# Kernel tuning notes

Hardware: AMD Instinct MI355X
Metric: run time of the kernel (lower is better)

The kernel has to match this reference:

```python
import jax, jax.numpy as jnp
import numpy as np

B, L = 2, 2048
D_MODEL = 512
KERNEL = 5
DILATIONS = (1, 2, 4, 8, 1, 2, 4, 8)
HEADS = len(DILATIONS)
HEAD_W = D_MODEL // HEADS
MODE = "center"


def _dilocal_content(x_bedl, kernel, dilations, mode):
    # x_bedl: (B, E, D, L). Returns content in layout (B, L, E, H, K, D),
    # matching LCSA's dilocal + transpose(-4,-1).transpose(-4,-2).transpose(-5,-4).
    Lx = x_bedl.shape[-1]
    per_head = []
    for d in dilations:
        P = (kernel - 1) * d
        if mode == "forward":
            pads = (P, 0)
        elif mode == "backward":
            pads = (0, P)
        else:  # center
            pads = (P // 2, P - P // 2)
        padded = jnp.pad(x_bedl, ((0, 0),) * (x_bedl.ndim - 1) + (pads,))
        win = jnp.stack([padded[..., k * d:k * d + Lx] for k in range(kernel)], axis=-2)
        per_head.append(win)
    c = jnp.stack(per_head, axis=-2)  # (B, E, D, K, H, L)
    return jnp.transpose(c, (0, 5, 1, 4, 3, 2))  # (B, L, E, H, K, D)


def setup_inputs() -> dict:
    key = jax.random.key(0)
    ks = jax.random.split(key, 6)
    s_in = 1.0 / np.sqrt(D_MODEL)
    s_out = 1.0 / np.sqrt(HEADS * HEAD_W)
    x = jax.random.normal(ks[0], (B, L, D_MODEL), jnp.float32)
    q_w = jax.random.normal(ks[1], (1, HEADS, 1, HEAD_W, D_MODEL), jnp.float32) * s_in
    q_b = jnp.zeros((1, HEADS, 1, HEAD_W), jnp.float32)
    k_w = jax.random.normal(ks[2], (1, HEADS, KERNEL, HEAD_W, D_MODEL), jnp.float32) * s_in
    k_b = jnp.zeros((1, HEADS, KERNEL, HEAD_W), jnp.float32)
    v_w = jax.random.normal(ks[3], (1, HEADS, KERNEL, HEAD_W, D_MODEL), jnp.float32) * s_in
    v_b = jnp.zeros((1, HEADS, KERNEL, HEAD_W), jnp.float32)
    o_w = jax.random.normal(ks[4], (1, D_MODEL, HEADS * HEAD_W), jnp.float32) * s_out
    o_b = jnp.zeros((1, D_MODEL), jnp.float32)
    return {"x": x, "q_w": q_w, "q_b": q_b, "k_w": k_w, "k_b": k_b,
            "v_w": v_w, "v_b": v_b, "o_w": o_w, "o_b": o_b}


def reference(x, q_w, q_b, k_w, k_b, v_w, v_b, o_w, o_b) -> jnp.ndarray:
    b, l, _ = x.shape
    # ensemble=None path: unsqueeze(-3) then transpose(-2,-1) -> (B, E=1, D, L)
    t = jnp.swapaxes(x[:, None, :, :], -2, -1)
    content = _dilocal_content(t, KERNEL, DILATIONS, MODE)  # (B, L, 1, H, K, D)
    # query uses kernel_width=1 (no padding, dilation irrelevant): (B, L, 1, H, 1, D)
    query = jnp.broadcast_to(x[:, :, None, None, None, :], (b, l, 1, HEADS, 1, D_MODEL))
    # per-(head, kernel-position) projections
    q = jnp.einsum('blehkd,ehkod->blehko', query, q_w) + q_b      # (B,L,1,H,1,O)
    k = jnp.einsum('blehkd,ehkod->blehko', content, k_w) + k_b    # (B,L,1,H,K,O)
    v = jnp.einsum('blehkd,ehkod->blehko', content, v_w) + v_b    # (B,L,1,H,K,O)
    logits = jnp.einsum('blehqo,blehko->blehqk', q, k)            # (B,L,1,H,1,K)
    score = jax.nn.softmax(logits, axis=-1)
    attn = jnp.einsum('blehqk,blehko->blehqo', score, v) / jnp.sqrt(jnp.float32(HEAD_W))
    attn = attn[..., 0, :]                                        # squeeze(-2) -> (B,L,1,H,O)
    flat = attn.reshape(b, l, 1, HEADS * HEAD_W)
    out = jnp.einsum('blef,eof->bleo', flat, o_w) + o_b           # (B,L,1,D)
    # transpose(-3,-2) then squeeze ensemble -> (B, L, D)
    return out[:, :, 0, :]
```

## Files before the change

kernel.cpp:

```cpp
#include <hip/hip_runtime.h>
#include <hip/hip_bf16.h>

using bf16 = __hip_bfloat16;
typedef __attribute__((ext_vector_type(8))) short short8;
typedef __attribute__((ext_vector_type(4))) float f32x4;

__device__ __constant__ int c_dil[8] = {1, 2, 4, 8, 1, 2, 4, 8};

__device__ inline void store1(float* p, float v) { *p = v; }
__device__ inline void store1(bf16* p, float v) { *p = __float2bfloat16(v); }

__device__ inline void gload_lds16(const void* g, void* l) {
    __builtin_amdgcn_global_load_lds(
        (const __attribute__((address_space(1))) unsigned int*)g,
        (__attribute__((address_space(3))) unsigned int*)l, 16, 0, 0);
}

template <int N> __device__ inline void vwait() {
    asm volatile("s_waitcnt vmcnt(%0)" :: "n"(N) : "memory");
    __builtin_amdgcn_sched_barrier(0);
}
__device__ inline void lgkm0_fence() {
    asm volatile("s_waitcnt lgkmcnt(0)" ::: "memory");
    __builtin_amdgcn_sched_barrier(0);
}
__device__ inline void barrier_pin() {
    __builtin_amdgcn_s_barrier();
    __builtin_amdgcn_sched_barrier(0);
}

__device__ inline unsigned short f2bf(float f) {
    const unsigned u = __float_as_uint(f);
    return (unsigned short)((u + 0x7fffu + ((u >> 16) & 1u)) >> 16);
}
__device__ inline float bf2f(unsigned short h) { return __uint_as_float(((unsigned)h) << 16); }

__device__ inline void conv_block(const float* __restrict__ src, bf16* __restrict__ dst,
                                  int ld, int mode, int idx) {
    const float4 v = *reinterpret_cast<const float4*>(src + idx);
    const int r = idx >> 9, c = idx & 511;
    bf16* d = dst + (size_t)r * ld + c;
    const float vv[4] = {v.x, v.y, v.z, v.w};
    ushort4 hi, lo;
    unsigned short* hp = &hi.x; unsigned short* lp = &lo.x;
#pragma unroll
    for (int j = 0; j < 4; ++j) {
        hp[j] = f2bf(vv[j]);
        lp[j] = f2bf(vv[j] - bf2f(hp[j]));
    }
    *reinterpret_cast<ushort4*>(d) = hi;
    if (mode == 1) *reinterpret_cast<ushort4*>(d + 512) = lo;
}

__global__ __launch_bounds__(256) void conv_all(
    const float* __restrict__ x,  const float* __restrict__ qw, const float* __restrict__ kw,
    const float* __restrict__ vw, const float* __restrict__ ow,
    const float* __restrict__ qb, const float* __restrict__ kb,
    bf16* A2, bf16* Wqk, bf16* Wv, bf16* Wo, float* bqk)
{
    const int b = blockIdx.x, t = threadIdx.x;
    if (b < 2048)       conv_block(x,  A2,                      1024, 1, (b * 256 + t) * 4);
    else if (b < 2304)  conv_block(qw, Wqk,                      512, 0, ((b - 2048) * 256 + t) * 4);
    else if (b < 3584)  conv_block(kw, Wqk + (size_t)512 * 512,  512, 0, ((b - 2304) * 256 + t) * 4);
    else if (b < 4864)  conv_block(vw, Wv,                       512, 0, ((b - 3584) * 256 + t) * 4);
    else if (b < 5120)  conv_block(ow, Wo,                       512, 0, ((b - 4864) * 256 + t) * 4);
    else { const int i = (b - 5120) * 256 + t; bqk[i] = (i < 512) ? qb[i] : kb[i - 512]; }
}

template <bool HILO>
__device__ __forceinline__ void run_gemm(
    short* smem,
    const bf16* __restrict__ A,
    const bf16* __restrict__ W,
    const float* __restrict__ bias,
    bf16* __restrict__ C, int ldc, int ncols,
    int bm, int bn)
{
    constexpr int NSTEPS = 16;
    short* Ahi = smem;
    short* Alo = smem + 8192;
    short* Bs  = smem + 16384;

    const int tid = threadIdx.x, wid = tid >> 6, lane = tid & 63;

    const int sslot = (((tid & 3) ^ ((tid >> 3) & 3)) << 4);
    const char* pAh = (const char*)A + (size_t)(bm + (tid >> 2)) * 2048 + sslot;
    const char* pB  = (const char*)W + (size_t)(bn + (tid >> 2)) * 1024 + sslot;

    auto stage = [&](int kt) {
        char* da = (char*)(Ahi + (kt & 1) * 4096);
        char* db = (char*)(Bs  + (kt & 1) * 6144);
        gload_lds16(pAh,          da + wid * 1024);
        gload_lds16(pAh + 131072, da + 4096 + wid * 1024);
        if (HILO) {
            char* dl = (char*)(Alo + (kt & 1) * 4096);
            gload_lds16(pAh + 1024,          dl + wid * 1024);
            gload_lds16(pAh + 1024 + 131072, dl + 4096 + wid * 1024);
        }
        gload_lds16(pB,           db + wid * 1024);
        gload_lds16(pB + 65536,   db + 4096 + wid * 1024);
        gload_lds16(pB + 131072,  db + 8192 + wid * 1024);
        pAh += 64; pB += 64;
    };

    f32x4 acc[4][6];
#pragma unroll
    for (int m = 0; m < 4; ++m)
#pragma unroll
        for (int n = 0; n < 6; ++n) acc[m][n] = f32x4{0.f, 0.f, 0.f, 0.f};

    const int lr16 = lane & 15;
    const int koff = (((lane >> 4) ^ ((lr16 >> 1) & 3)) << 3);
    const int wrM = wid >> 1, wcN = wid & 1;
    const int arow0 = wrM * 64 + lr16;
    const int brow0 = wcN * 96 + lr16;

    stage(0);

    for (int kt = 0; kt < NSTEPS; ++kt) {
        vwait<0>();
        barrier_pin();

        const short* ah = Ahi + (kt & 1) * 4096;
        const short* al = Alo + (kt & 1) * 4096;
        const short* bb = Bs  + (kt & 1) * 6144;
        short8 fh[4], fl[4], bw[6];
#pragma unroll
        for (int m = 0; m < 4; ++m) {
            fh[m] = *(const short8*)&ah[(arow0 + m * 16) * 32 + koff];
            if (HILO) fl[m] = *(const short8*)&al[(arow0 + m * 16) * 32 + koff];
        }
#pragma unroll
        for (int n = 0; n < 6; ++n)
            bw[n] = *(const short8*)&bb[(brow0 + n * 16) * 32 + koff];
        lgkm0_fence();
        barrier_pin();

        if (kt + 1 < NSTEPS) stage(kt + 1);

        __builtin_amdgcn_s_setprio(1);
#pragma unroll
        for (int m = 0; m < 4; ++m)
#pragma unroll
            for (int n = 0; n < 6; ++n)
                acc[m][n] = __builtin_amdgcn_mfma_f32_16x16x32_bf16(fh[m], bw[n], acc[m][n], 0, 0, 0);
        if (HILO) {
#pragma unroll
            for (int m = 0; m < 4; ++m)
#pragma unroll
                for (int n = 0; n < 6; ++n)
                    acc[m][n] = __builtin_amdgcn_mfma_f32_16x16x32_bf16(fl[m], bw[n], acc[m][n], 0, 0, 0);
        }
        __builtin_amdgcn_s_setprio(0);
    }

    const int r4 = (lane >> 4) * 4;
#pragma unroll
    for (int m = 0; m < 4; ++m) {
#pragma unroll
        for (int n = 0; n < 6; ++n) {
            const int col = bn + wcN * 96 + n * 16 + lr16;
            if (col < ncols) {
                const float bv = bias[col];
#pragma unroll
                for (int jj = 0; jj < 4; ++jj) {
                    const int row = bm + wrM * 64 + m * 16 + r4 + jj;
                    store1(C + (size_t)row * ldc + col, acc[m][n][jj] + bv);
                }
            }
        }
    }
}

__global__ __launch_bounds__(256, 2) void gemm_qkv(
    const bf16* __restrict__ A,
    const bf16* __restrict__ Wqk, const float* __restrict__ bqk, bf16* __restrict__ PQK,
    const bf16* __restrict__ Wv,  const float* __restrict__ vb,  bf16* __restrict__ PV)
{
    __shared__ short smem[28672];
    const int b = blockIdx.x;
    if (b < 512) {
        const int xcd = b & 7, i = b >> 3;
        const int by = xcd * 4 + (i & 3), bx = i >> 2;
        run_gemm<true>(smem, A, Wqk, bqk, PQK, 3072, 3072, by * 128, bx * 192);
    } else {
        const int v = b - 512;
        const int xcd = v & 7, i = v >> 3;
        const int by = xcd * 4 + (i & 3), bx = i >> 2;
        run_gemm<false>(smem, A, Wv, vb, PV, 2560, 2560, by * 128, bx * 192);
    }
}

template <int BN, typename TC>
__global__ __launch_bounds__(256) void gemm128(
    const bf16* __restrict__ A, int lda, int cw, int rpx,
    const bf16* __restrict__ W0, int ldw0, const float* __restrict__ b0,
    TC* __restrict__ C0, int ldc0, int nt0, int nx0)
{
    constexpr int NF = BN / 32;
    constexpr int NLOAD = (BN == 128) ? 4 : 3;
    __shared__ short As[4][128 * 32];
    __shared__ short Bs[4][BN * 32];

    const int tid = threadIdx.x, wid = tid >> 6, lane = tid & 63;

    const int xcd = (int)blockIdx.x & 7;
    const int i   = (int)blockIdx.x >> 3;
    const int grp = rpx * cw;
    const int cc = i / grp, w2 = i % grp;
    const int rr = w2 / cw, c = w2 % cw;
    const int bx = cc * cw + c;
    const int by = xcd * rpx + rr;

    const int bm = by * 128;
    const int bn = bx * BN;
    const int nsteps = nt0;

    const int srow = lane >> 2;
    const int ssw  = (((lane & 3) ^ ((lane >> 3) & 3)) << 4);
    const char* pA0 = (const char*)A + (size_t)(bm + wid * 16 + srow) * lda * 2 + ssw;
    const char* pA1 = pA0 + (size_t)64 * lda * 2;
    const char* pB0 = (const char*)W0 + (size_t)(bn + wid * 16 + srow) * ldw0 * 2 + ssw;

    f32x4 acc[4][NF];
#pragma unroll
    for (int m = 0; m < 4; ++m)
#pragma unroll
        for (int n = 0; n < NF; ++n) acc[m][n] = f32x4{0.f, 0.f, 0.f, 0.f};

    const int lr16 = lane & 15;
    const int wsw8 = (((lane >> 4) ^ ((lr16 >> 1) & 3)) << 3);
    const int wr = wid >> 1, wc = wid & 1;
    int offA[4], offB[NF];
#pragma unroll
    for (int m = 0; m < 4; ++m) offA[m] = (wr * 4 + m) * 512 + lr16 * 32 + wsw8;
#pragma unroll
    for (int n = 0; n < NF; ++n) offB[n] = (wc * NF + n) * 512 + lr16 * 32 + wsw8;

    auto stage = [&](int buf) {
        gload_lds16(pA0, (char*)As[buf] + wid * 1024);
        gload_lds16(pA1, (char*)As[buf] + (wid + 4) * 1024);
        gload_lds16(pB0, (char*)Bs[buf] + wid * 1024);
        pA0 += 64; pA1 += 64; pB0 += 64;
    };

    stage(0);
    stage(1);
    stage(2);

    for (int s = 0; s < nsteps; ++s) {
        const int cur = s & 3;
        if (s + 3 < nsteps) {
            stage((s + 3) & 3);
            vwait<3 * NLOAD>();
        } else if (s + 2 < nsteps) {
            vwait<2 * NLOAD>();
        } else if (s + 1 < nsteps) {
            vwait<NLOAD>();
        } else {
            vwait<0>();
        }
        barrier_pin();

        short8 af[4], bw[NF];
#pragma unroll
        for (int m = 0; m < 4; ++m)
            af[m] = *(const short8*)&As[cur][offA[m]];
#pragma unroll
        for (int n = 0; n < NF; ++n)
            bw[n] = *(const short8*)&Bs[cur][offB[n]];

        __builtin_amdgcn_s_setprio(1);
#pragma unroll
        for (int m = 0; m < 4; ++m)
#pragma unroll
            for (int n = 0; n < NF; ++n)
                acc[m][n] = __builtin_amdgcn_mfma_f32_16x16x32_bf16(af[m], bw[n], acc[m][n], 0, 0, 0);
        __builtin_amdgcn_s_setprio(0);

        barrier_pin();
    }

    const int r4 = (lane >> 4) * 4;
#pragma unroll
    for (int m = 0; m < 4; ++m) {
#pragma unroll
        for (int n = 0; n < NF; ++n) {
            const int col = bn + wc * (NF * 16) + n * 16 + lr16;
            const float bv = b0[col];
#pragma unroll
            for (int jj = 0; jj < 4; ++jj) {
                const int row = bm + wr * 64 + m * 16 + r4 + jj;
                store1(C0 + (size_t)row * ldc0 + col, acc[m][n][jj] + bv);
            }
        }
    }
}

__global__ __launch_bounds__(256) void attn_k(
    const bf16* __restrict__ PQK, const bf16* __restrict__ PV, bf16* __restrict__ Aout)
{
    const int lane = threadIdx.x & 63;
    const int wave = threadIdx.x >> 6;
    const int task = blockIdx.x * 4 + wave;
    const int h  = task & 7;
    const int bl = task >> 3;
    const int l  = bl & 2047;
    const int d  = c_dil[h];

    const float q = __bfloat162float(PQK[(size_t)bl * 3072 + h * 64 + lane]);

    float logits[5], vvals[5];
#pragma unroll
    for (int kk = 0; kk < 5; ++kk) {
        const int pos = l + (kk - 2) * d;
        const bool ok = (pos >= 0) && (pos < 2048);
        float kv = 0.f, vv = 0.f;
        if (ok) {
            const size_t rb = (size_t)(bl - l + pos);
            kv = __bfloat162float(PQK[rb * 3072 + 512 + (h * 5 + kk) * 64 + lane]);
            vv = __bfloat162float(PV[rb * 2560 + (h * 5 + kk) * 64 + lane]);
        }
        vvals[kk] = vv;
        float lg = q * kv;
#pragma unroll
        for (int s = 32; s; s >>= 1) lg += __shfl_xor(lg, s);
        logits[kk] = lg;
    }

    float mx = logits[0];
#pragma unroll
    for (int kk = 1; kk < 5; ++kk) mx = fmaxf(mx, logits[kk]);
    float e[5], ssum = 0.f;
#pragma unroll
    for (int kk = 0; kk < 5; ++kk) { e[kk] = __expf(logits[kk] - mx); ssum += e[kk]; }
    float acc = 0.f;
#pragma unroll
    for (int kk = 0; kk < 5; ++kk) acc += e[kk] * vvals[kk];
    acc *= 0.125f / ssum;

    Aout[(size_t)bl * 512 + h * 64 + lane] = __float2bfloat16(acc);
}

extern "C" void kernel_launch(void* const* d_in, const int* in_sizes, int n_in,
                              void* d_out, int out_size, void* d_ws, size_t ws_size,
                              hipStream_t stream)
{
    const float* x   = (const float*)d_in[0];
    const float* q_w = (const float*)d_in[1];
    const float* q_b = (const float*)d_in[2];
    const float* k_w = (const float*)d_in[3];
    const float* k_b = (const float*)d_in[4];
    const float* v_w = (const float*)d_in[5];
    const float* v_b = (const float*)d_in[6];
    const float* o_w = (const float*)d_in[7];
    const float* o_b = (const float*)d_in[8];
    float* out = (float*)d_out;

    const int M = 4096;

    char* p = (char*)d_ws;
    bf16* A2  = (bf16*)p;  p += (size_t)M * 1024 * 2;
    bf16* Wqk = (bf16*)p;  p += (size_t)3072 * 512 * 2;
    bf16* Wv  = (bf16*)p;  p += (size_t)2688 * 512 * 2;
    bf16* Wo  = (bf16*)p;  p += (size_t)512 * 512 * 2;
    float* bqk = (float*)p; p += 3072 * 4;
    bf16* PQK = (bf16*)p;  p += (size_t)M * 3072 * 2;
    bf16* PV  = (bf16*)p;
    bf16* Aout = A2;

    conv_all<<<dim3(5132), dim3(256), 0, stream>>>(x, q_w, k_w, v_w, o_w, q_b, k_b,
                                                   A2, Wqk, Wv, Wo, bqk);
    gemm_qkv<<<dim3(960), dim3(256), 0, stream>>>(A2, Wqk, bqk, PQK, Wv, v_b, PV);
    attn_k<<<dim3(8192), dim3(256), 0, stream>>>(PQK, PV, Aout);
    gemm128<64, float><<<dim3(256), dim3(256), 0, stream>>>(
        Aout, 512, 8, 4,
        Wo, 512, o_b, out, 512, 16, 8);
}
```

Measured before the change: 81.06 us.

## Vectorize attention to one wave per row and drop redundant GEMM barriers

The attention kernel now assigns one wave per sequence position covering all eight heads, with each lane handling 8 contiguous outputs. This turns scalar bf16 loads and stores into 16-byte vector accesses and cuts the logit reduction from a 6-step to a 3-step shuffle. Both GEMM main loops also drop a block barrier: the next-stage prefetch is issued after the LDS fragment reads and relies on the barrier at the top of the next iteration for buffer reuse safety. This reduces sync stalls, but the hazard analysis becomes subtler and each lane holds more registers.

```diff
diff --git a/kernel.cpp b/kernel.cpp
--- a/kernel.cpp
+++ b/kernel.cpp
@@ -18,10 +18,6 @@
 
 template <int N> __device__ inline void vwait() {
     asm volatile("s_waitcnt vmcnt(%0)" :: "n"(N) : "memory");
-    __builtin_amdgcn_sched_barrier(0);
-}
-__device__ inline void lgkm0_fence() {
-    asm volatile("s_waitcnt lgkmcnt(0)" ::: "memory");
     __builtin_amdgcn_sched_barrier(0);
 }
 __device__ inline void barrier_pin() {
@@ -133,8 +129,6 @@
 #pragma unroll
         for (int n = 0; n < 6; ++n)
             bw[n] = *(const short8*)&bb[(brow0 + n * 16) * 32 + koff];
-        lgkm0_fence();
-        barrier_pin();
 
         if (kt + 1 < NSTEPS) stage(kt + 1);
 
@@ -250,16 +244,9 @@
 
     for (int s = 0; s < nsteps; ++s) {
         const int cur = s & 3;
-        if (s + 3 < nsteps) {
-            stage((s + 3) & 3);
-            vwait<3 * NLOAD>();
-        } else if (s + 2 < nsteps) {
-            vwait<2 * NLOAD>();
-        } else if (s + 1 < nsteps) {
-            vwait<NLOAD>();
-        } else {
-            vwait<0>();
-        }
+        if (s + 2 < nsteps)      vwait<2 * NLOAD>();
+        else if (s + 1 < nsteps) vwait<NLOAD>();
+        else                     vwait<0>();
         barrier_pin();
 
         short8 af[4], bw[NF];
@@ -269,6 +256,8 @@
 #pragma unroll
         for (int n = 0; n < NF; ++n)
             bw[n] = *(const short8*)&Bs[cur][offB[n]];
+
+        if (s + 3 < nsteps) stage((s + 3) & 3);
 
         __builtin_amdgcn_s_setprio(1);
 #pragma unroll
@@ -277,8 +266,6 @@
             for (int n = 0; n < NF; ++n)
                 acc[m][n] = __builtin_amdgcn_mfma_f32_16x16x32_bf16(af[m], bw[n], acc[m][n], 0, 0, 0);
         __builtin_amdgcn_s_setprio(0);
-
-        barrier_pin();
     }
 
     const int r4 = (lane >> 4) * 4;
@@ -302,30 +289,44 @@
 {
     const int lane = threadIdx.x & 63;
     const int wave = threadIdx.x >> 6;
-    const int task = blockIdx.x * 4 + wave;
-    const int h  = task & 7;
-    const int bl = task >> 3;
+    const int bl = blockIdx.x * 4 + wave;
     const int l  = bl & 2047;
+    const int h  = lane >> 3;
     const int d  = c_dil[h];
-
-    const float q = __bfloat162float(PQK[(size_t)bl * 3072 + h * 64 + lane]);
-
-    float logits[5], vvals[5];
+    const int o8 = (lane & 7) * 8;
+
+    float q[8];
+    {
+        const short8 qv = *(const short8*)&PQK[(size_t)bl * 3072 + lane * 8];
+#pragma unroll
+        for (int i = 0; i < 8; ++i) q[i] = bf2f((unsigned short)qv[i]);
+    }
+
+    float logits[5];
+    float vv[5][8];
 #pragma unroll
     for (int kk = 0; kk < 5; ++kk) {
         const int pos = l + (kk - 2) * d;
         const bool ok = (pos >= 0) && (pos < 2048);
-        float kv = 0.f, vv = 0.f;
+        float s = 0.f;
         if (ok) {
             const size_t rb = (size_t)(bl - l + pos);
-            kv = __bfloat162float(PQK[rb * 3072 + 512 + (h * 5 + kk) * 64 + lane]);
-            vv = __bfloat162float(PV[rb * 2560 + (h * 5 + kk) * 64 + lane]);
-        }
-        vvals[kk] = vv;
-        float lg = q * kv;
-#pragma unroll
-        for (int s = 32; s; s >>= 1) lg += __shfl_xor(lg, s);
-        logits[kk] = lg;
+            const int coff = h * 320 + kk * 64 + o8;
+            const short8 kv = *(const short8*)&PQK[rb * 3072 + 512 + coff];
+            const short8 vvv = *(const short8*)&PV[rb * 2560 + coff];
+#pragma unroll
+            for (int i = 0; i < 8; ++i) {
+                s = fmaf(bf2f((unsigned short)kv[i]), q[i], s);
+                vv[kk][i] = bf2f((unsigned short)vvv[i]);
+            }
+        } else {
+#pragma unroll
+            for (int i = 0; i < 8; ++i) vv[kk][i] = 0.f;
+        }
+        s += __shfl_xor(s, 1);
+        s += __shfl_xor(s, 2);
+        s += __shfl_xor(s, 4);
+        logits[kk] = s;
     }
 
     float mx = logits[0];
@@ -334,12 +335,17 @@
     float e[5], ssum = 0.f;
 #pragma unroll
     for (int kk = 0; kk < 5; ++kk) { e[kk] = __expf(logits[kk] - mx); ssum += e[kk]; }
-    float acc = 0.f;
-#pragma unroll
-    for (int kk = 0; kk < 5; ++kk) acc += e[kk] * vvals[kk];
-    acc *= 0.125f / ssum;
-
-    Aout[(size_t)bl * 512 + h * 64 + lane] = __float2bfloat16(acc);
+    const float sc = 0.125f / ssum;
+
+    short8 outv;
+#pragma unroll
+    for (int i = 0; i < 8; ++i) {
+        float a = 0.f;
+#pragma unroll
+        for (int kk = 0; kk < 5; ++kk) a = fmaf(e[kk], vv[kk][i], a);
+        outv[i] = (short)f2bf(a * sc);
+    }
+    *(short8*)&Aout[(size_t)bl * 512 + lane * 8] = outv;
 }
 
 extern "C" void kernel_launch(void* const* d_in, const int* in_sizes, int n_in,
@@ -372,7 +378,7 @@
     conv_all<<<dim3(5132), dim3(256), 0, stream>>>(x, q_w, k_w, v_w, o_w, q_b, k_b,
                                                    A2, Wqk, Wv, Wo, bqk);
     gemm_qkv<<<dim3(960), dim3(256), 0, stream>>>(A2, Wqk, bqk, PQK, Wv, v_b, PV);
-    attn_k<<<dim3(8192), dim3(256), 0, stream>>>(PQK, PV, Aout);
+    attn_k<<<dim3(2048), dim3(256), 0, stream>>>(PQK, PV, Aout);
     gemm128<64, float><<<dim3(256), dim3(256), 0, stream>>>(
         Aout, 512, 8, 4,
         Wo, 512, o_b, out, 512, 16, 8);
```

Result: faster. 77.60 us (-4.3%).
